# Kernel tuning notes

Measured on AMD Instinct MI355X. Metric: run time of the kernel, lower is better.

## Reference

```python
import jax, jax.numpy as jnp
import numpy as np

N_HEADS = 16
NEG_INF = -1e9


def _apply_rope(xq, xk, cos, sin):
    # xq, xk: [B, S, H, hd]; cos/sin: [S, hd//2]
    def rot(t):
        B, S, H, hd = t.shape
        t = t.reshape(B, S, H, hd // 2, 2)
        t0, t1 = t[..., 0], t[..., 1]
        c = cos[None, :, None, :]
        s = sin[None, :, None, :]
        o0 = t0 * c - t1 * s
        o1 = t0 * s + t1 * c
        return jnp.stack([o0, o1], axis=-1).reshape(B, S, H, hd)
    return rot(xq), rot(xk)


def setup_inputs() -> dict:
    key = jax.random.key(0)
    ks = jax.random.split(key, 7)
    B, S, D = 2, 2048, 2048
    hd = D // N_HEADS
    return {
        "x": jax.random.normal(ks[0], (B, S, D), dtype=jnp.float32),
        "freqs_cos": jax.random.uniform(ks[1], (S, hd // 2), dtype=jnp.float32),
        "freqs_sin": jax.random.uniform(ks[2], (S, hd // 2), dtype=jnp.float32),
        "wq": jax.random.normal(ks[3], (D, D), dtype=jnp.float32) * 0.02,
        "wk": jax.random.normal(ks[4], (D, D), dtype=jnp.float32) * 0.02,
        "wv": jax.random.normal(ks[5], (D, D), dtype=jnp.float32) * 0.02,
        "wo": jax.random.normal(ks[6], (D, D), dtype=jnp.float32) * 0.02,
    }


def reference(x, freqs_cos, freqs_sin, wq, wk, wv, wo):
    B, S, D = x.shape
    H = N_HEADS
    hd = D // H

    # projections (torch Linear: y = x @ W.T)
    xq = (x @ wq.T).reshape(B, S, H, hd)
    xk = (x @ wk.T).reshape(B, S, H, hd)
    xv = (x @ wv.T).reshape(B, S, H, hd)

    xq, xk = _apply_rope(xq, xk, freqs_cos, freqs_sin)

    # [B, H, S, hd]
    q = xq.transpose(0, 2, 1, 3)
    k = xk.transpose(0, 2, 1, 3)
    v = xv.transpose(0, 2, 1, 3)

    scores = jnp.einsum("bhqd,bhkd->bhqk", q, k) / jnp.sqrt(jnp.float32(hd))
    causal = jnp.triu(jnp.full((S, S), NEG_INF, dtype=scores.dtype), k=1)
    scores = scores + causal[None, None]
    probs = jax.nn.softmax(scores.astype(jnp.float32), axis=-1).astype(q.dtype)

    out = jnp.einsum("bhqk,bhkd->bhqd", probs, v)
    out = out.transpose(0, 2, 1, 3).reshape(B, S, D)
    return out @ wo.T
```

## Files before the change

kernel.cpp:

```cpp
#include <hip/hip_runtime.h>
#include <hip/hip_bf16.h>
#include <math.h>

typedef __attribute__((ext_vector_type(8))) short short8;
typedef __attribute__((ext_vector_type(4))) float f32x4;
typedef unsigned short ushort_t;

__device__ __forceinline__ ushort_t f2bf(float f) {
    union { float f; unsigned u; } v; v.f = f;
    unsigned r = v.u + 0x7FFF + ((v.u >> 16) & 1);
    return (ushort_t)(r >> 16);
}
__device__ __forceinline__ float bf2f(short s) {
    union { unsigned u; float f; } v; v.u = ((unsigned)(ushort_t)s) << 16;
    return v.f;
}

__global__ void cvt_kernel(const float* __restrict__ src, ushort_t* __restrict__ dst, int n8) {
    int i = blockIdx.x * blockDim.x + threadIdx.x;
    int stride = gridDim.x * blockDim.x;
    for (; i < n8; i += stride) {
        const float4* s = reinterpret_cast<const float4*>(src) + (size_t)i * 2;
        float4 a = s[0], b = s[1];
        short8 o;
        o[0] = (short)f2bf(a.x); o[1] = (short)f2bf(a.y);
        o[2] = (short)f2bf(a.z); o[3] = (short)f2bf(a.w);
        o[4] = (short)f2bf(b.x); o[5] = (short)f2bf(b.y);
        o[6] = (short)f2bf(b.z); o[7] = (short)f2bf(b.w);
        reinterpret_cast<short8*>(dst)[i] = o;
    }
}

__global__ void cvtw_kernel(const float* __restrict__ w0, const float* __restrict__ w1,
                            const float* __restrict__ w2, const float* __restrict__ w3,
                            ushort_t* __restrict__ dst, int dd8) {
    int i = blockIdx.x * blockDim.x + threadIdx.x;
    int stride = gridDim.x * blockDim.x;
    const int total = dd8 * 4;
    for (; i < total; i += stride) {
        int which = i / dd8;
        int off = i - which * dd8;
        const float* src = (which == 0) ? w0 : (which == 1) ? w1 : (which == 2) ? w2 : w3;
        const float4* s = reinterpret_cast<const float4*>(src) + (size_t)off * 2;
        float4 a = s[0], b = s[1];
        short8 o;
        o[0] = (short)f2bf(a.x); o[1] = (short)f2bf(a.y);
        o[2] = (short)f2bf(a.z); o[3] = (short)f2bf(a.w);
        o[4] = (short)f2bf(b.x); o[5] = (short)f2bf(b.y);
        o[6] = (short)f2bf(b.z); o[7] = (short)f2bf(b.w);
        reinterpret_cast<short8*>(dst)[i] = o;
    }
}

template<int OUT_MODE>
__global__ __launch_bounds__(256) void gemm_nt(const ushort_t* __restrict__ A,
                                               const ushort_t* __restrict__ Bw,
                                               void* __restrict__ Cout,
                                               int M, int N, int K) {
    __shared__ __align__(16) ushort_t As[2 * 128 * 32];
    __shared__ __align__(16) ushort_t Bs[2 * 128 * 32];
    const int t = threadIdx.x;
    const int wid = t >> 6, lane = t & 63;
    const int wm = wid >> 1, wn = wid & 1;
    const int lr = lane & 15, lg = lane >> 4;

    const int ntc = N >> 7;
    const int nwg = (M >> 7) * ntc;
    const int bid = blockIdx.y * gridDim.x + blockIdx.x;
    const int cpx = nwg >> 3;
    const int swz = (bid & 7) * cpx + (bid >> 3);
    const int m0 = (swz / ntc) * 128, n0 = (swz % ntc) * 128;

    f32x4 acc[4][4] = {};

    const int sh0 = wid * 1024 + lane * 8;
    const int sh1 = sh0 + 512;
    const int r0 = sh0 >> 5, c0 = sh0 & 31;
    const int r1 = sh1 >> 5, c1 = sh1 & 31;

    const ushort_t* gA0 = A + (long)(m0 + r0) * K + c0;
    const ushort_t* gA1 = A + (long)(m0 + r1) * K + c1;
    const ushort_t* gB0 = Bw + (long)(n0 + r0) * K + c0;
    const ushort_t* gB1 = Bw + (long)(n0 + r1) * K + c1;

    auto stage = [&](int k0, int nb) {
        ushort_t* as = As + nb * 4096;
        ushort_t* bs = Bs + nb * 4096;
        __builtin_amdgcn_global_load_lds((const __attribute__((address_space(1))) unsigned int*)(gA0 + k0),
                                         (__attribute__((address_space(3))) unsigned int*)(as + sh0), 16, 0, 0);
        __builtin_amdgcn_global_load_lds((const __attribute__((address_space(1))) unsigned int*)(gA1 + k0),
                                         (__attribute__((address_space(3))) unsigned int*)(as + sh1), 16, 0, 0);
        __builtin_amdgcn_global_load_lds((const __attribute__((address_space(1))) unsigned int*)(gB0 + k0),
                                         (__attribute__((address_space(3))) unsigned int*)(bs + sh0), 16, 0, 0);
        __builtin_amdgcn_global_load_lds((const __attribute__((address_space(1))) unsigned int*)(gB1 + k0),
                                         (__attribute__((address_space(3))) unsigned int*)(bs + sh1), 16, 0, 0);
    };

    const int nt = K >> 5;
    stage(0, 0);
    __syncthreads();
    int cur = 0;

    for (int ti = 0; ti < nt; ++ti) {
        if (ti + 1 < nt) stage((ti + 1) << 5, cur ^ 1);
        const ushort_t* as = As + cur * 4096;
        const ushort_t* bs = Bs + cur * 4096;
        short8 af[4], bfr[4];
        #pragma unroll
        for (int m = 0; m < 4; ++m)
            af[m] = *reinterpret_cast<const short8*>(&as[(wm * 64 + m * 16 + lr) * 32 + lg * 8]);
        #pragma unroll
        for (int n = 0; n < 4; ++n)
            bfr[n] = *reinterpret_cast<const short8*>(&bs[(wn * 64 + n * 16 + lr) * 32 + lg * 8]);
        #pragma unroll
        for (int m = 0; m < 4; ++m)
            #pragma unroll
            for (int n = 0; n < 4; ++n)
                acc[m][n] = __builtin_amdgcn_mfma_f32_16x16x32_bf16(af[m], bfr[n], acc[m][n], 0, 0, 0);
        __syncthreads();
        cur ^= 1;
    }

    #pragma unroll
    for (int m = 0; m < 4; ++m) {
        #pragma unroll
        for (int n = 0; n < 4; ++n) {
            const int col = n0 + wn * 64 + n * 16 + lr;
            #pragma unroll
            for (int r = 0; r < 4; ++r) {
                const int row = m0 + wm * 64 + m * 16 + lg * 4 + r;
                float v = acc[m][n][r];
                if (OUT_MODE == 0) {
                    ((float*)Cout)[(long)row * N + col] = v;
                } else {
                    const int which = col >> 11;
                    const int h = (col >> 7) & 15;
                    const int d = col & 127;
                    const int b = row >> 11, s = row & 2047;
                    ((ushort_t*)Cout)[(long)which * M * 2048 +
                                      (((long)(b * 16 + h)) * 2048 + s) * 128 + d] = f2bf(v);
                }
            }
        }
    }
}

__global__ void rope_kernel(ushort_t* __restrict__ X, const float* __restrict__ fc,
                            const float* __restrict__ fs, int total8) {
    int i = blockIdx.x * blockDim.x + threadIdx.x;
    if (i >= total8) return;
    const int s_idx = (i >> 4) & 2047;
    const int i0 = (i & 15) * 4;
    const long base = (long)i * 8;
    short8 v = *reinterpret_cast<const short8*>(X + base);
    short8 o;
    #pragma unroll
    for (int p = 0; p < 4; ++p) {
        float c  = fc[(long)s_idx * 64 + i0 + p];
        float sn = fs[(long)s_idx * 64 + i0 + p];
        float x0 = bf2f(v[2 * p]), x1 = bf2f(v[2 * p + 1]);
        o[2 * p]     = (short)f2bf(x0 * c - x1 * sn);
        o[2 * p + 1] = (short)f2bf(x0 * sn + x1 * c);
    }
    *reinterpret_cast<short8*>(X + base) = o;
}

__global__ void vtrans_kernel(const ushort_t* __restrict__ Vp, ushort_t* __restrict__ Vt,
                              int S) {
    const int bh = blockIdx.y;
    const int s0 = blockIdx.x * 16 + ((threadIdx.x >> 7) * 8);
    const int d = threadIdx.x & 127;
    const ushort_t* src = Vp + (long)bh * S * 128;
    short8 o;
    #pragma unroll
    for (int i = 0; i < 8; ++i)
        o[i] = (short)src[(long)(s0 + i) * 128 + d];
    *reinterpret_cast<short8*>(Vt + ((long)bh * 128 + d) * S + s0) = o;
}

__global__ __launch_bounds__(256, 3) void attn_kernel(const ushort_t* __restrict__ Qp,
                                                      const ushort_t* __restrict__ Kp,
                                                      const ushort_t* __restrict__ Vtg,
                                                      ushort_t* __restrict__ O,
                                                      int S, int H) {
    __shared__ __align__(16) ushort_t Ks[64][136];
    __shared__ __align__(16) ushort_t Vs[128][72];
    __shared__ __align__(16) ushort_t Pl[4][16][72];
    const int t = threadIdx.x, wid = t >> 6, lane = t & 63;
    const int lr = lane & 15, lg = lane >> 4;
    const int bh = blockIdx.y;
    const int b = bh / H, h = bh % H;
    const ushort_t* Qh = Qp + (long)bh * S * 128;
    const ushort_t* Kh = Kp + (long)bh * S * 128;
    const ushort_t* Vth = Vtg + (long)bh * 128 * S;
    const int nq = S / 64;
    const float scale = 0.08838834764831845f;

    const int ksr = t >> 2;
    const int ksc = (t & 3) * 32;
    const int vsr = t & 127;
    const int vsc = (t >> 7) * 32;

    for (int qsel = 0; qsel < 2; ++qsel) {
        const int qt = qsel ? (nq - 1 - blockIdx.x) : blockIdx.x;
        const int qb0 = qt * 64;

        const int qrow = qb0 + wid * 16 + lr;
        short8 qf[4];
        #pragma unroll
        for (int kk = 0; kk < 4; ++kk)
            qf[kk] = *reinterpret_cast<const short8*>(Qh + (long)qrow * 128 + kk * 32 + lg * 8);

        f32x4 oacc[8] = {};
        float mrow[4], lsum[4];
        #pragma unroll
        for (int r = 0; r < 4; ++r) { mrow[r] = -INFINITY; lsum[r] = 0.f; }

        const int nkt = qt + 1;

        short8 kreg[4], vreg[4];
        {
            const ushort_t* kgp = Kh + t * 32;
            const ushort_t* vgp = Vth + (long)vsr * S + vsc;
            #pragma unroll
            for (int j = 0; j < 4; ++j) kreg[j] = *reinterpret_cast<const short8*>(kgp + j * 8);
            #pragma unroll
            for (int j = 0; j < 4; ++j) vreg[j] = *reinterpret_cast<const short8*>(vgp + j * 8);
        }

        for (int kt = 0; kt < nkt; ++kt) {
            const int kv0 = kt * 64;
            __syncthreads();
            #pragma unroll
            for (int j = 0; j < 4; ++j)
                *reinterpret_cast<short8*>(&Ks[ksr][ksc + j * 8]) = kreg[j];
            #pragma unroll
            for (int j = 0; j < 4; ++j)
                *reinterpret_cast<short8*>(&Vs[vsr][vsc + j * 8]) = vreg[j];
            __syncthreads();
            if (kt + 1 < nkt) {
                const ushort_t* kgp = Kh + (long)(kv0 + 64) * 128 + t * 32;
                const ushort_t* vgp = Vth + (long)vsr * S + kv0 + 64 + vsc;
                #pragma unroll
                for (int j = 0; j < 4; ++j) kreg[j] = *reinterpret_cast<const short8*>(kgp + j * 8);
                #pragma unroll
                for (int j = 0; j < 4; ++j) vreg[j] = *reinterpret_cast<const short8*>(vgp + j * 8);
            }

            f32x4 sacc[4] = {};
            #pragma unroll
            for (int kk = 0; kk < 4; ++kk) {
                #pragma unroll
                for (int n = 0; n < 4; ++n) {
                    short8 kf = *reinterpret_cast<const short8*>(&Ks[n * 16 + lr][kk * 32 + lg * 8]);
                    sacc[n] = __builtin_amdgcn_mfma_f32_16x16x32_bf16(qf[kk], kf, sacc[n], 0, 0, 0);
                }
            }
            float sv[4][4];
            const int myq = qb0 + wid * 16 + lg * 4;
            #pragma unroll
            for (int n = 0; n < 4; ++n) {
                int kcol = kv0 + n * 16 + lr;
                #pragma unroll
                for (int r = 0; r < 4; ++r) {
                    float xv = sacc[n][r] * scale;
                    sv[n][r] = (kcol > myq + r) ? -1e9f : xv;
                }
            }
            float alpha[4];
            #pragma unroll
            for (int r = 0; r < 4; ++r) {
                float mx = fmaxf(fmaxf(sv[0][r], sv[1][r]), fmaxf(sv[2][r], sv[3][r]));
                #pragma unroll
                for (int off = 1; off < 16; off <<= 1)
                    mx = fmaxf(mx, __shfl_xor(mx, off));
                float mnew = fmaxf(mrow[r], mx);
                alpha[r] = __expf(mrow[r] - mnew);
                float ts = 0.f;
                #pragma unroll
                for (int n = 0; n < 4; ++n) {
                    float p = __expf(sv[n][r] - mnew);
                    sv[n][r] = p;
                    ts += p;
                }
                #pragma unroll
                for (int off = 1; off < 16; off <<= 1)
                    ts += __shfl_xor(ts, off);
                lsum[r] = lsum[r] * alpha[r] + ts;
                mrow[r] = mnew;
            }
            #pragma unroll
            for (int f = 0; f < 8; ++f)
                #pragma unroll
                for (int r = 0; r < 4; ++r)
                    oacc[f][r] *= alpha[r];
            #pragma unroll
            for (int n = 0; n < 4; ++n)
                #pragma unroll
                for (int r = 0; r < 4; ++r)
                    Pl[wid][lg * 4 + r][n * 16 + lr] = f2bf(sv[n][r]);
            __asm volatile("" ::: "memory");
            short8 pf[2];
            #pragma unroll
            for (int ks = 0; ks < 2; ++ks)
                pf[ks] = *reinterpret_cast<const short8*>(&Pl[wid][lr][ks * 32 + lg * 8]);
            #pragma unroll
            for (int f = 0; f < 8; ++f) {
                #pragma unroll
                for (int ks = 0; ks < 2; ++ks) {
                    short8 vf = *reinterpret_cast<const short8*>(&Vs[f * 16 + lr][ks * 32 + lg * 8]);
                    oacc[f] = __builtin_amdgcn_mfma_f32_16x16x32_bf16(pf[ks], vf, oacc[f], 0, 0, 0);
                }
            }
        }
        float inv[4];
        #pragma unroll
        for (int r = 0; r < 4; ++r) inv[r] = 1.f / lsum[r];
        ushort_t* Oh = O + (long)b * S * 2048 + h * 128;
        #pragma unroll
        for (int f = 0; f < 8; ++f) {
            #pragma unroll
            for (int r = 0; r < 4; ++r) {
                int row = qb0 + wid * 16 + lg * 4 + r;
                int col = f * 16 + lr;
                Oh[(long)row * 2048 + col] = f2bf(oacc[f][r] * inv[r]);
            }
        }
    }
}

extern "C" void kernel_launch(void* const* d_in, const int* in_sizes, int n_in,
                              void* d_out, int out_size, void* d_ws, size_t ws_size,
                              hipStream_t stream) {
    const float* x  = (const float*)d_in[0];
    const float* fc = (const float*)d_in[1];
    const float* fs = (const float*)d_in[2];
    const float* wq = (const float*)d_in[3];
    const float* wk = (const float*)d_in[4];
    const float* wv = (const float*)d_in[5];
    const float* wo = (const float*)d_in[6];
    float* out = (float*)d_out;

    const int B = 2, S = 2048, D = 2048, H = 16;
    const int M = B * S;
    const size_t MD = (size_t)M * D;
    const size_t DD = (size_t)D * D;

    char* ws = (char*)d_ws;
    ushort_t* xbf = (ushort_t*)ws;
    ushort_t* wqb = (ushort_t*)(ws + MD * 2);
    ushort_t* wob = wqb + 3 * DD;
    ushort_t* qp  = wqb + 4 * DD;
    ushort_t* kp  = qp + MD;
    ushort_t* vp  = kp + MD;
    ushort_t* vtg   = xbf;
    ushort_t* attnb = vp;

    cvt_kernel<<<2048, 256, 0, stream>>>(x, xbf, (int)(MD / 8));
    cvtw_kernel<<<2048, 256, 0, stream>>>(wq, wk, wv, wo, wqb, (int)(DD / 8));

    dim3 gq(6144 / 128, M / 128);
    gemm_nt<1><<<gq, 256, 0, stream>>>(xbf, wqb, qp, M, 3 * D, D);

    const int total8 = (int)(2 * MD / 8);
    rope_kernel<<<(total8 + 255) / 256, 256, 0, stream>>>(qp, fc, fs, total8);

    dim3 gv(S / 16, B * H);
    vtrans_kernel<<<gv, 256, 0, stream>>>(vp, vtg, S);
    dim3 ga(S / 128, B * H);
    attn_kernel<<<ga, 256, 0, stream>>>(qp, kp, vtg, attnb, S, H);

    dim3 gg(D / 128, M / 128);
    gemm_nt<0><<<gg, 256, 0, stream>>>(attnb, wob, out, M, D, D);
}
```

Before: 318.5 us.

## Replace QKV projection GEMM with 256x256-tile, 8-wave pipelined MFMA kernel

Adds a new QKV projection kernel that uses 256x256 output tiles, 512 threads and 128KB of dynamic LDS. It loads directly from global memory into LDS with double buffering and interleaves LDS reads, async stage loads and MFMA quadrants, using barriers and setprio to schedule them. The larger tile raises arithmetic intensity and data reuse per workgroup compared with the 128x128 kernel. In exchange it uses much more LDS and registers, so occupancy drops and the launch has fewer workgroups (384). The epilogue writes bf16 output directly in the head-major layout.

```diff
diff --git a/kernel.cpp b/kernel.cpp
--- a/kernel.cpp
+++ b/kernel.cpp
@@ -52,6 +52,174 @@
     }
 }
 
+__global__ __launch_bounds__(512, 2) void gemm256_qkv(const ushort_t* __restrict__ A,
+                                                      const ushort_t* __restrict__ Bw,
+                                                      ushort_t* __restrict__ Cout,
+                                                      int M, int N, int K) {
+    extern __shared__ __align__(16) ushort_t lds[];
+    ushort_t* As = lds;
+    ushort_t* Bs = lds + 32768;
+    const int t = threadIdx.x;
+    const int wid = t >> 6, lane = t & 63;
+    const int wr = wid >> 2, wc = wid & 3;
+    const int lr = lane & 15, lg = lane >> 4;
+
+    const int ntc = N >> 8;
+    const int nwg = (M >> 8) * ntc;
+    const int bid = blockIdx.y * gridDim.x + blockIdx.x;
+    const int cpx = nwg >> 3;
+    const int swz = (bid & 7) * cpx + (bid >> 3);
+    const int m0 = (swz / ntc) * 256, n0 = (swz % ntc) * 256;
+
+    f32x4 acc[8][4] = {};
+
+    const int r0 = t >> 3;
+    const int c0 = (t & 7) ^ (r0 & 7);
+    const ushort_t* gA = A + (long)(m0 + r0) * K + c0 * 8;
+    const ushort_t* gB = Bw + (long)(n0 + r0) * K + c0 * 8;
+
+    int aoffE[2];
+    aoffE[0] = lr * 64 + (((0 + lg) ^ (lr & 7)) << 3);
+    aoffE[1] = lr * 64 + (((4 + lg) ^ (lr & 7)) << 3);
+
+    const int nt = K >> 6;
+
+#define STAGE_A(X, h) do { const int p_ = (X) & 1;                                             \
+    __builtin_amdgcn_global_load_lds((const __attribute__((address_space(1))) unsigned int*)   \
+        (gA + (long)((h) * 128) * K + (X) * 64),                                               \
+        (__attribute__((address_space(3))) unsigned int*)(As + (p_ * 2 + (h)) * 8192 + t * 8), \
+        16, 0, 0);                                                                             \
+    __builtin_amdgcn_global_load_lds((const __attribute__((address_space(1))) unsigned int*)   \
+        (gA + (long)((h) * 128 + 64) * K + (X) * 64),                                          \
+        (__attribute__((address_space(3))) unsigned int*)(As + (p_ * 2 + (h)) * 8192 + 4096 + t * 8), \
+        16, 0, 0); } while (0)
+
+#define STAGE_B(X, h) do { const int p_ = (X) & 1;                                             \
+    __builtin_amdgcn_global_load_lds((const __attribute__((address_space(1))) unsigned int*)   \
+        (gB + (long)((h) * 128) * K + (X) * 64),                                               \
+        (__attribute__((address_space(3))) unsigned int*)(Bs + (p_ * 2 + (h)) * 8192 + t * 8), \
+        16, 0, 0);                                                                             \
+    __builtin_amdgcn_global_load_lds((const __attribute__((address_space(1))) unsigned int*)   \
+        (gB + (long)((h) * 128 + 64) * K + (X) * 64),                                          \
+        (__attribute__((address_space(3))) unsigned int*)(Bs + (p_ * 2 + (h)) * 8192 + 4096 + t * 8), \
+        16, 0, 0); } while (0)
+
+    STAGE_A(0, 0); STAGE_A(0, 1); STAGE_B(0, 0); STAGE_B(0, 1);
+    STAGE_A(1, 0); STAGE_B(1, 0); STAGE_B(1, 1);
+    asm volatile("s_waitcnt vmcnt(6)" ::: "memory");
+    __builtin_amdgcn_s_barrier();
+
+    short8 ar[4][2], br0[2][2], br1[2][2];
+
+    for (int U = 0; U < nt; ++U) {
+        const int b = U & 1;
+        const int Asb = (b * 2 + wr) * 8192;
+        const int Bcb = (b * 2 + (wc >> 1)) * 8192 + (wc & 1) * 4096;
+
+        #pragma unroll
+        for (int m = 0; m < 4; ++m)
+            #pragma unroll
+            for (int ks = 0; ks < 2; ++ks)
+                ar[m][ks] = *reinterpret_cast<const short8*>(&As[Asb + m * 1024 + aoffE[ks]]);
+        #pragma unroll
+        for (int n = 0; n < 2; ++n)
+            #pragma unroll
+            for (int ks = 0; ks < 2; ++ks)
+                br0[n][ks] = *reinterpret_cast<const short8*>(&Bs[Bcb + n * 1024 + aoffE[ks]]);
+        if (U + 1 < nt) STAGE_A(U + 1, 1);
+        asm volatile("" ::: "memory");
+        __builtin_amdgcn_s_barrier();
+        __builtin_amdgcn_s_setprio(1);
+        #pragma unroll
+        for (int m = 0; m < 4; ++m)
+            #pragma unroll
+            for (int n = 0; n < 2; ++n)
+                #pragma unroll
+                for (int ks = 0; ks < 2; ++ks)
+                    acc[m][n] = __builtin_amdgcn_mfma_f32_16x16x32_bf16(ar[m][ks], br0[n][ks], acc[m][n], 0, 0, 0);
+        __builtin_amdgcn_s_setprio(0);
+        asm volatile("" ::: "memory");
+        __builtin_amdgcn_s_barrier();
+
+        #pragma unroll
+        for (int n = 0; n < 2; ++n)
+            #pragma unroll
+            for (int ks = 0; ks < 2; ++ks)
+                br1[n][ks] = *reinterpret_cast<const short8*>(&Bs[Bcb + 2048 + n * 1024 + aoffE[ks]]);
+        asm volatile("" ::: "memory");
+        __builtin_amdgcn_s_barrier();
+        __builtin_amdgcn_s_setprio(1);
+        #pragma unroll
+        for (int m = 0; m < 4; ++m)
+            #pragma unroll
+            for (int n = 0; n < 2; ++n)
+                #pragma unroll
+                for (int ks = 0; ks < 2; ++ks)
+                    acc[m][2 + n] = __builtin_amdgcn_mfma_f32_16x16x32_bf16(ar[m][ks], br1[n][ks], acc[m][2 + n], 0, 0, 0);
+        __builtin_amdgcn_s_setprio(0);
+        asm volatile("" ::: "memory");
+        __builtin_amdgcn_s_barrier();
+
+        #pragma unroll
+        for (int m = 0; m < 4; ++m)
+            #pragma unroll
+            for (int ks = 0; ks < 2; ++ks)
+                ar[m][ks] = *reinterpret_cast<const short8*>(&As[Asb + 4096 + m * 1024 + aoffE[ks]]);
+        if (U + 2 < nt) STAGE_B(U + 2, 0);
+        asm volatile("" ::: "memory");
+        __builtin_amdgcn_s_barrier();
+        __builtin_amdgcn_s_setprio(1);
+        #pragma unroll
+        for (int m = 0; m < 4; ++m)
+            #pragma unroll
+            for (int n = 0; n < 2; ++n)
+                #pragma unroll
+                for (int ks = 0; ks < 2; ++ks)
+                    acc[4 + m][2 + n] = __builtin_amdgcn_mfma_f32_16x16x32_bf16(ar[m][ks], br1[n][ks], acc[4 + m][2 + n], 0, 0, 0);
+        __builtin_amdgcn_s_setprio(0);
+        asm volatile("" ::: "memory");
+        __builtin_amdgcn_s_barrier();
+
+        if (U + 2 < nt) { STAGE_A(U + 2, 0); STAGE_B(U + 2, 1); }
+        asm volatile("" ::: "memory");
+        __builtin_amdgcn_s_barrier();
+        __builtin_amdgcn_s_setprio(1);
+        #pragma unroll
+        for (int m = 0; m < 4; ++m)
+            #pragma unroll
+            for (int n = 0; n < 2; ++n)
+                #pragma unroll
+                for (int ks = 0; ks < 2; ++ks)
+                    acc[4 + m][n] = __builtin_amdgcn_mfma_f32_16x16x32_bf16(ar[m][ks], br0[n][ks], acc[4 + m][n], 0, 0, 0);
+        __builtin_amdgcn_s_setprio(0);
+        if (U < nt - 2) {
+            asm volatile("s_waitcnt vmcnt(6)" ::: "memory");
+        } else if (U == nt - 2) {
+            asm volatile("s_waitcnt vmcnt(0)" ::: "memory");
+        }
+        __builtin_amdgcn_s_barrier();
+    }
+#undef STAGE_A
+#undef STAGE_B
+
+    #pragma unroll
+    for (int m = 0; m < 8; ++m) {
+        #pragma unroll
+        for (int n = 0; n < 4; ++n) {
+            const int col = n0 + wc * 64 + n * 16 + lr;
+            const int which = col >> 11;
+            const int h = (col >> 7) & 15;
+            const int d = col & 127;
+            #pragma unroll
+            for (int r = 0; r < 4; ++r) {
+                const int row = m0 + wr * 128 + m * 16 + lg * 4 + r;
+                const int bb = row >> 11, s = row & 2047;
+                Cout[(long)which * M * 2048 + (((long)(bb * 16 + h)) * 2048 + s) * 128 + d] = f2bf(acc[m][n][r]);
+            }
+        }
+    }
+}
+
 template<int OUT_MODE>
 __global__ __launch_bounds__(256) void gemm_nt(const ushort_t* __restrict__ A,
                                                const ushort_t* __restrict__ Bw,
@@ -359,8 +527,8 @@
     cvt_kernel<<<2048, 256, 0, stream>>>(x, xbf, (int)(MD / 8));
     cvtw_kernel<<<2048, 256, 0, stream>>>(wq, wk, wv, wo, wqb, (int)(DD / 8));
 
-    dim3 gq(6144 / 128, M / 128);
-    gemm_nt<1><<<gq, 256, 0, stream>>>(xbf, wqb, qp, M, 3 * D, D);
+    dim3 gq(6144 / 256, M / 256);
+    gemm256_qkv<<<gq, 512, 131072, stream>>>(xbf, wqb, qp, M, 3 * D, D);
 
     const int total8 = (int)(2 * MD / 8);
     rope_kernel<<<(total8 + 255) / 256, 256, 0, stream>>>(qp, fc, fs, total8);
```

Measured after the change: 322.9 us. No clear change (+1.4%).

## Add 256x256-tile QKV GEMM with direct-to-LDS loads and staged pipelining

Applied to the files above, without the earlier changes.

Replaces the 128x128-tile QKV projection GEMM with a new 512-thread kernel that computes 256x256 output tiles. It streams global data straight into LDS with global_load_lds, double-buffers the tiles and interleaves quarter-tile MFMA groups with barriers and wait counts. The goal is more data reuse per byte loaded and better overlap of loads with matrix math. Costs are 128KB of dynamic LDS per block, higher register pressure, and a grid of only 384 blocks. It also reorders the PV MFMA loop in attention so the ks loop is outermost.

```diff
diff --git a/kernel.cpp b/kernel.cpp
--- a/kernel.cpp
+++ b/kernel.cpp
@@ -52,6 +52,165 @@
     }
 }
 
+__global__ __launch_bounds__(512, 2) void gemm256_qkv(const ushort_t* __restrict__ A,
+                                                      const ushort_t* __restrict__ Bw,
+                                                      ushort_t* __restrict__ Cout,
+                                                      int M, int N, int K) {
+    extern __shared__ __align__(16) ushort_t lds[];
+    ushort_t* As = lds;
+    ushort_t* Bs = lds + 32768;
+    const int t = threadIdx.x;
+    const int wid = t >> 6, lane = t & 63;
+    const int wr = wid >> 2, wc = wid & 3;
+    const int lr = lane & 15, lg = lane >> 4;
+
+    const int ntc = N >> 8;
+    const int nwg = (M >> 8) * ntc;
+    const int bid = blockIdx.y * gridDim.x + blockIdx.x;
+    const int cpx = nwg >> 3;
+    const int swz = (bid & 7) * cpx + (bid >> 3);
+    const int m0 = (swz / ntc) * 256, n0 = (swz % ntc) * 256;
+
+    f32x4 acc[8][4] = {};
+
+    const int r0 = t >> 3;
+    const int c0 = (t & 7) ^ (r0 & 7);
+    const ushort_t* gA = A + (long)(m0 + r0) * K + c0 * 8;
+    const ushort_t* gB = Bw + (long)(n0 + r0) * K + c0 * 8;
+
+    int aoffE[2];
+    aoffE[0] = lr * 64 + (((0 + lg) ^ (lr & 7)) << 3);
+    aoffE[1] = lr * 64 + (((4 + lg) ^ (lr & 7)) << 3);
+
+    const int nt = K >> 6;
+
+#define STAGE_A(X, h) do { const int p_ = (X) & 1;                                             \
+    __builtin_amdgcn_global_load_lds((const __attribute__((address_space(1))) unsigned int*)   \
+        (gA + (long)((h) * 128) * K + (X) * 64),                                               \
+        (__attribute__((address_space(3))) unsigned int*)(As + (p_ * 2 + (h)) * 8192 + t * 8), \
+        16, 0, 0);                                                                             \
+    __builtin_amdgcn_global_load_lds((const __attribute__((address_space(1))) unsigned int*)   \
+        (gA + (long)((h) * 128 + 64) * K + (X) * 64),                                          \
+        (__attribute__((address_space(3))) unsigned int*)(As + (p_ * 2 + (h)) * 8192 + 4096 + t * 8), \
+        16, 0, 0); } while (0)
+
+#define STAGE_B(X, h) do { const int p_ = (X) & 1;                                             \
+    __builtin_amdgcn_global_load_lds((const __attribute__((address_space(1))) unsigned int*)   \
+        (gB + (long)((h) * 128) * K + (X) * 64),                                               \
+        (__attribute__((address_space(3))) unsigned int*)(Bs + (p_ * 2 + (h)) * 8192 + t * 8), \
+        16, 0, 0);                                                                             \
+    __builtin_amdgcn_global_load_lds((const __attribute__((address_space(1))) unsigned int*)   \
+        (gB + (long)((h) * 128 + 64) * K + (X) * 64),                                          \
+        (__attribute__((address_space(3))) unsigned int*)(Bs + (p_ * 2 + (h)) * 8192 + 4096 + t * 8), \
+        16, 0, 0); } while (0)
+
+#define MIDSYNC() do {                                             \
+    asm volatile("" ::: "memory");                                 \
+    __builtin_amdgcn_s_barrier();                                  \
+    asm volatile("s_waitcnt lgkmcnt(0)" ::: "memory");             \
+    __builtin_amdgcn_sched_barrier(0); } while (0)
+
+#define ENDBAR() do {                                              \
+    asm volatile("" ::: "memory");                                 \
+    __builtin_amdgcn_s_barrier(); } while (0)
+
+#define MFMA_Q(AROW, BCOL, AR, BR) do {                            \
+    __builtin_amdgcn_s_setprio(1);                                 \
+    _Pragma("unroll")                                              \
+    for (int ks = 0; ks < 2; ++ks)                                 \
+        _Pragma("unroll")                                          \
+        for (int m = 0; m < 4; ++m)                                \
+            _Pragma("unroll")                                      \
+            for (int n = 0; n < 2; ++n)                            \
+                acc[(AROW) + m][(BCOL) + n] =                      \
+                    __builtin_amdgcn_mfma_f32_16x16x32_bf16((AR)[m][ks], (BR)[n][ks], acc[(AROW) + m][(BCOL) + n], 0, 0, 0); \
+    __builtin_amdgcn_s_setprio(0); } while (0)
+
+#define KTILE(U, BUF) do {                                                                     \
+    const int Asb = ((BUF) * 2 + wr) * 8192;                                                   \
+    const int Bcb = ((BUF) * 2 + (wc >> 1)) * 8192 + (wc & 1) * 4096;                          \
+                                          \
+    _Pragma("unroll")                                                                          \
+    for (int m = 0; m < 4; ++m)                                                                \
+        _Pragma("unroll")                                                                      \
+        for (int ks = 0; ks < 2; ++ks)                                                         \
+            ar[m][ks] = *reinterpret_cast<const short8*>(&As[Asb + m * 1024 + aoffE[ks]]);     \
+    _Pragma("unroll")                                                                          \
+    for (int n = 0; n < 2; ++n)                                                                \
+        _Pragma("unroll")                                                                      \
+        for (int ks = 0; ks < 2; ++ks)                                                         \
+            br0[n][ks] = *reinterpret_cast<const short8*>(&Bs[Bcb + n * 1024 + aoffE[ks]]);    \
+    if ((U) + 1 < nt) STAGE_A((U) + 1, 1);                                                     \
+    MIDSYNC();                                                                                 \
+    MFMA_Q(0, 0, ar, br0);                                                                     \
+    ENDBAR();                                                                                  \
+                                                                  \
+    _Pragma("unroll")                                                                          \
+    for (int n = 0; n < 2; ++n)                                                                \
+        _Pragma("unroll")                                                                      \
+        for (int ks = 0; ks < 2; ++ks)                                                         \
+            br1[n][ks] = *reinterpret_cast<const short8*>(&Bs[Bcb + 2048 + n * 1024 + aoffE[ks]]); \
+    MIDSYNC();                                                                                 \
+    MFMA_Q(0, 2, ar, br1);                                                                     \
+    ENDBAR();                                                                                  \
+                                                 \
+    _Pragma("unroll")                                                                          \
+    for (int m = 0; m < 4; ++m)                                                                \
+        _Pragma("unroll")                                                                      \
+        for (int ks = 0; ks < 2; ++ks)                                                         \
+            ar[m][ks] = *reinterpret_cast<const short8*>(&As[Asb + 4096 + m * 1024 + aoffE[ks]]); \
+    if ((U) + 2 < nt) STAGE_B((U) + 2, 0);                                                     \
+    MIDSYNC();                                                                                 \
+    MFMA_Q(4, 2, ar, br1);                                                                     \
+    ENDBAR();                                                                                  \
+                                  \
+    if ((U) + 2 < nt) { STAGE_A((U) + 2, 0); STAGE_B((U) + 2, 1); }                            \
+    asm volatile("" ::: "memory");                                                             \
+    __builtin_amdgcn_s_barrier();                                                              \
+    MFMA_Q(4, 0, ar, br0);                                                                     \
+    if ((U) < nt - 2) {                                                                        \
+        asm volatile("s_waitcnt vmcnt(6)" ::: "memory");                                       \
+    } else if ((U) == nt - 2) {                                                                \
+        asm volatile("s_waitcnt vmcnt(0)" ::: "memory");                                       \
+    }                                                                                          \
+    __builtin_amdgcn_s_barrier(); } while (0)
+
+    STAGE_A(0, 0); STAGE_A(0, 1); STAGE_B(0, 0); STAGE_B(0, 1);
+    STAGE_A(1, 0); STAGE_B(1, 0); STAGE_B(1, 1);
+    asm volatile("s_waitcnt vmcnt(6)" ::: "memory");
+    __builtin_amdgcn_s_barrier();
+
+    short8 ar[4][2], br0[2][2], br1[2][2];
+
+    for (int U = 0; U < nt; U += 2) {
+        KTILE(U, 0);
+        KTILE(U + 1, 1);
+    }
+#undef KTILE
+#undef MFMA_Q
+#undef ENDBAR
+#undef MIDSYNC
+#undef STAGE_A
+#undef STAGE_B
+
+    #pragma unroll
+    for (int m = 0; m < 8; ++m) {
+        #pragma unroll
+        for (int n = 0; n < 4; ++n) {
+            const int col = n0 + wc * 64 + n * 16 + lr;
+            const int which = col >> 11;
+            const int h = (col >> 7) & 15;
+            const int d = col & 127;
+            #pragma unroll
+            for (int r = 0; r < 4; ++r) {
+                const int row = m0 + wr * 128 + m * 16 + lg * 4 + r;
+                const int bb = row >> 11, s = row & 2047;
+                Cout[(long)which * M * 2048 + (((long)(bb * 16 + h)) * 2048 + s) * 128 + d] = f2bf(acc[m][n][r]);
+            }
+        }
+    }
+}
+
 template<int OUT_MODE>
 __global__ __launch_bounds__(256) void gemm_nt(const ushort_t* __restrict__ A,
                                                const ushort_t* __restrict__ Bw,
@@ -305,9 +464,9 @@
             for (int ks = 0; ks < 2; ++ks)
                 pf[ks] = *reinterpret_cast<const short8*>(&Pl[wid][lr][ks * 32 + lg * 8]);
             #pragma unroll
-            for (int f = 0; f < 8; ++f) {
-                #pragma unroll
-                for (int ks = 0; ks < 2; ++ks) {
+            for (int ks = 0; ks < 2; ++ks) {
+                #pragma unroll
+                for (int f = 0; f < 8; ++f) {
                     short8 vf = *reinterpret_cast<const short8*>(&Vs[f * 16 + lr][ks * 32 + lg * 8]);
                     oacc[f] = __builtin_amdgcn_mfma_f32_16x16x32_bf16(pf[ks], vf, oacc[f], 0, 0, 0);
                 }
@@ -359,8 +518,8 @@
     cvt_kernel<<<2048, 256, 0, stream>>>(x, xbf, (int)(MD / 8));
     cvtw_kernel<<<2048, 256, 0, stream>>>(wq, wk, wv, wo, wqb, (int)(DD / 8));
 
-    dim3 gq(6144 / 128, M / 128);
-    gemm_nt<1><<<gq, 256, 0, stream>>>(xbf, wqb, qp, M, 3 * D, D);
+    dim3 gq(6144 / 256, M / 256);
+    gemm256_qkv<<<gq, 512, 131072, stream>>>(xbf, wqb, qp, M, 3 * D, D);
 
     const int total8 = (int)(2 * MD / 8);
     rope_kernel<<<(total8 + 255) / 256, 256, 0, stream>>>(qp, fc, fs, total8);
```

After: 322.9 us. No clear change (+1.4%).
